# Performance work log

Hardware: AMD Instinct MI355X
Metric: run time of the kernel (lower is better)

The kernel has to match this reference:

```python
import jax, jax.numpy as jnp
import numpy as np


def setup_inputs() -> dict:
    key = jax.random.key(0)
    kx, kf = jax.random.split(key)
    x = jax.random.normal(kx, (4, 8192, 1024), dtype=jnp.float32)
    filt = jax.random.normal(kf, (2048,), dtype=jnp.float32)
    return {"x": x, "filt": filt}


def reference(x, filt):
    # x: (batch, seq, dim); filt: (filter_length,)
    batch, seq, dim = x.shape
    L = filt.shape[0]
    pad = seq + L - 1
    # long-sequence FFT branch (seq > 64)
    xt = jnp.swapaxes(x, 1, 2)                 # (b, d, s)
    fx = jnp.fft.rfft(xt, n=pad, axis=-1)      # (b, d, pad//2+1) complex
    ff = jnp.fft.rfft(filt[::-1], n=pad)       # (pad//2+1,) complex
    conv = jnp.fft.irfft(fx * ff, n=pad, axis=-1)  # (b, d, pad)
    conv = conv[:, :, L - 1:L - 1 + seq]       # valid region, length seq
    return jnp.swapaxes(conv, 1, 2)            # (b, s, d)
```

## Files before the change

kernel.cpp:

```cpp
#include <hip/hip_runtime.h>

typedef unsigned short u16;
typedef unsigned int   u32;

#define BATCH 4
#define SEQ   8192
#define DIM   1024
#define FL    2048
#define TROW  10240

#define BM 512
#define BN 64
#define BK 64
#define NSTAGE 40
#define WOFF 64
#define NW   2272
#define WIN_HI 2174

typedef float  f32x4  __attribute__((ext_vector_type(4)));
typedef __bf16 bf16x8 __attribute__((ext_vector_type(8)));
typedef short  s16x8  __attribute__((ext_vector_type(8)));

typedef const __attribute__((address_space(1))) void* gas_t;
typedef __attribute__((address_space(3))) void* las_t;

__device__ __forceinline__ u16 f2bf(float f) {
  u32 u = __float_as_uint(f);
  u += 0x7fffu + ((u >> 16) & 1u);
  return (u16)(u >> 16);
}

__global__ __launch_bounds__(256) void k_transpose(const float* __restrict__ x,
                                                   u16* __restrict__ xT) {
  __shared__ __align__(16) u16 sm[64 * 66];
  const int bid = blockIdx.x;
  const int tb = bid % (TROW / 64);
  const int db = (bid / (TROW / 64)) % (DIM / 64);
  const int b  = bid / ((TROW / 64) * (DIM / 64));
  const int t0 = tb * 64, d0 = db * 64;
  const int tid = threadIdx.x;

  const int c4 = tid & 15;
  const int lt = tid >> 4;
  const float* xb = x + (size_t)b * SEQ * DIM + d0 + c4 * 4;
  #pragma unroll
  for (int s = 0; s < 64; s += 16) {
    const int tl = lt + s;
    const int t = t0 + tl;
    float4 v = make_float4(0.f, 0.f, 0.f, 0.f);
    if (t < SEQ) v = *(const float4*)(xb + (size_t)t * DIM);
    u32 p0 = (u32)f2bf(v.x) | ((u32)f2bf(v.y) << 16);
    u32 p1 = (u32)f2bf(v.z) | ((u32)f2bf(v.w) << 16);
    u32* dst = (u32*)&sm[tl * 66 + c4 * 4];
    dst[0] = p0;
    dst[1] = p1;
  }
  __syncthreads();
  const int q  = tid & 7;
  const int dl = tid >> 3;
  u16* xo = xT + ((size_t)b * DIM + d0) * TROW + t0 + 8 * q;
  #pragma unroll
  for (int s = 0; s < 2; ++s) {
    const int d = dl + 32 * s;
    u32 w[4];
    #pragma unroll
    for (int h = 0; h < 4; ++h) {
      w[h] = (u32)sm[(8 * q + 2 * h) * 66 + d] |
             ((u32)sm[(8 * q + 2 * h + 1) * 66 + d] << 16);
    }
    *(uint4*)(xo + (size_t)d * TROW) = *(const uint4*)w;
  }
}

__global__ __launch_bounds__(256, 2) void k_conv(const u16* __restrict__ xT,
                                                 const float* __restrict__ filt,
                                                 float* __restrict__ out) {
  __shared__ __align__(16) u16 Wb[NW * 8];
  __shared__ __align__(16) u16 Xs[2][BN * BK];

  const int bid = blockIdx.x;
  const int tb = bid & 15;
  const int db = (bid >> 4) & 15;
  const int b  = bid >> 8;
  const int t0 = tb * BM;
  const int d0 = db * BN;

  const int tid  = threadIdx.x;
  const int wid  = tid >> 6;
  const int lane = tid & 63;
  const int quad = lane >> 4;
  const int lq   = lane & 15;
  const int Tw   = wid * 128;

  for (int w = tid; w < NW; w += 256) {
    const int base = w - WOFF;
    u32 pk[4];
    #pragma unroll
    for (int h = 0; h < 4; ++h) {
      const int i0 = base + 2 * h;
      const int i1 = i0 + 1;
      const float v0 = (i0 >= 0 && i0 < FL) ? filt[i0] : 0.f;
      const float v1 = (i1 >= 0 && i1 < FL) ? filt[i1] : 0.f;
      pk[h] = (u32)f2bf(v0) | ((u32)f2bf(v1) << 16);
    }
    u32* dst = (u32*)&Wb[w * 8];
    dst[0] = pk[0]; dst[1] = pk[1]; dst[2] = pk[2]; dst[3] = pk[3];
  }

  const u16* xrow = xT + ((size_t)b * DIM + d0) * TROW + t0;
  const int p0 = wid * 128 + lane;
  const int p1 = p0 + 64;
  const int ds0 = p0 >> 3, kc0 = (p0 & 7) ^ (ds0 & 7);
  const int ds1 = p1 >> 3, kc1 = (p1 & 7) ^ (ds1 & 7);
  const u16* gp0 = xrow + (size_t)ds0 * TROW + kc0 * 8;
  const u16* gp1 = xrow + (size_t)ds1 * TROW + kc1 * 8;

  f32x4 acc[8][4];
  const f32x4 fz = {0.f, 0.f, 0.f, 0.f};
  #pragma unroll
  for (int i = 0; i < 8; ++i)
    #pragma unroll
    for (int j = 0; j < 4; ++j) acc[i][j] = fz;

  const s16x8 sz = {0, 0, 0, 0, 0, 0, 0, 0};
  bf16x8 roll0 = __builtin_bit_cast(bf16x8, sz);
  bf16x8 roll1 = roll0, roll2 = roll0, roll3 = roll0, roll4 = roll0, roll5 = roll0;

  const int wconst = quad * 8 - Tw - lq + WOFF;
  const int kkLo = Tw - 31;
  const int kkHi = Tw + WIN_HI;

  {
    u16* nb = &Xs[0][wid * 1024];
    __builtin_amdgcn_global_load_lds((gas_t)gp0, (las_t)nb, 16, 0, 0);
    __builtin_amdgcn_global_load_lds((gas_t)gp1, (las_t)(nb + 512), 16, 0, 0);
  }

  for (int st = 0; st < NSTAGE; ++st) {
    __syncthreads();
    if (st + 1 < NSTAGE) {
      const int kkn = (st + 1) * BK;
      u16* nb = &Xs[(st + 1) & 1][wid * 1024];
      __builtin_amdgcn_global_load_lds((gas_t)(gp0 + kkn), (las_t)nb, 16, 0, 0);
      __builtin_amdgcn_global_load_lds((gas_t)(gp1 + kkn), (las_t)(nb + 512), 16, 0, 0);
    }
    const u16* Xc = &Xs[st & 1][0];
    const int kk0 = st * BK;
    #pragma unroll
    for (int half = 0; half < 2; ++half) {
      const int kk = kk0 + half * 32;
      if (kk >= kkLo && kk <= kkHi) {
        bf16x8 bfr[4];
        #pragma unroll
        for (int nt = 0; nt < 4; ++nt) {
          const int dl = nt * 16 + lq;
          const int kc = (half * 4 + quad) ^ (dl & 7);
          bfr[nt] = *(const bf16x8*)&Xc[(dl * 8 + kc) * 8];
        }
        const int w0 = kk + wconst;
        const bf16x8 a0 = *(const bf16x8*)&Wb[w0 * 8];
        const bf16x8 a1 = *(const bf16x8*)&Wb[(w0 - 16) * 8];
        #pragma unroll
        for (int nt = 0; nt < 4; ++nt) {
          acc[0][nt] = __builtin_amdgcn_mfma_f32_16x16x32_bf16(a0,    bfr[nt], acc[0][nt], 0, 0, 0);
          acc[1][nt] = __builtin_amdgcn_mfma_f32_16x16x32_bf16(a1,    bfr[nt], acc[1][nt], 0, 0, 0);
          acc[2][nt] = __builtin_amdgcn_mfma_f32_16x16x32_bf16(roll0, bfr[nt], acc[2][nt], 0, 0, 0);
          acc[3][nt] = __builtin_amdgcn_mfma_f32_16x16x32_bf16(roll1, bfr[nt], acc[3][nt], 0, 0, 0);
          acc[4][nt] = __builtin_amdgcn_mfma_f32_16x16x32_bf16(roll2, bfr[nt], acc[4][nt], 0, 0, 0);
          acc[5][nt] = __builtin_amdgcn_mfma_f32_16x16x32_bf16(roll3, bfr[nt], acc[5][nt], 0, 0, 0);
          acc[6][nt] = __builtin_amdgcn_mfma_f32_16x16x32_bf16(roll4, bfr[nt], acc[6][nt], 0, 0, 0);
          acc[7][nt] = __builtin_amdgcn_mfma_f32_16x16x32_bf16(roll5, bfr[nt], acc[7][nt], 0, 0, 0);
        }
        roll5 = roll3; roll4 = roll2; roll3 = roll1; roll2 = roll0;
        roll1 = a1; roll0 = a0;
      }
    }
  }

  float* ob = out + ((size_t)b * SEQ + t0 + Tw) * DIM + d0;
  #pragma unroll
  for (int mt = 0; mt < 8; ++mt) {
    #pragma unroll
    for (int nt = 0; nt < 4; ++nt) {
      #pragma unroll
      for (int r = 0; r < 4; ++r) {
        ob[(size_t)(mt * 16 + quad * 4 + r) * DIM + nt * 16 + lq] = acc[mt][nt][r];
      }
    }
  }
}

extern "C" void kernel_launch(void* const* d_in, const int* in_sizes, int n_in,
                              void* d_out, int out_size, void* d_ws, size_t ws_size,
                              hipStream_t stream) {
  const float* x    = (const float*)d_in[0];
  const float* filt = (const float*)d_in[1];
  float* out = (float*)d_out;
  u16* xT = (u16*)d_ws;
  (void)in_sizes; (void)n_in; (void)out_size; (void)ws_size;

  k_transpose<<<BATCH * (TROW / 64) * (DIM / 64), 256, 0, stream>>>(x, xT);
  k_conv<<<BATCH * 16 * 16, 256, 0, stream>>>(xT, filt, out);
}
```

Measured before the change: 344.6 us.

## Load B fragments directly from global into registers, drop LDS staging and barriers

Replaces the LDS double-buffered global_load_lds pipeline for the transposed input with per-wave direct global loads into registers, software-pipelined two steps ahead. Each wave now iterates only over its own 68 valid k-steps instead of checking a window across the whole block range, removing per-stage __syncthreads and LDS reads. MFMA bursts are wrapped in s_setprio. The risk is that global loads now expose latency and 16-byte row-strided accesses per lane may coalesce less well than the shared staging did.

```diff
diff --git a/kernel.cpp b/kernel.cpp
--- a/kernel.cpp
+++ b/kernel.cpp
@@ -11,18 +11,13 @@
 
 #define BM 512
 #define BN 64
-#define BK 64
-#define NSTAGE 40
+#define NSTEP 68
 #define WOFF 64
 #define NW   2272
-#define WIN_HI 2174
 
 typedef float  f32x4  __attribute__((ext_vector_type(4)));
 typedef __bf16 bf16x8 __attribute__((ext_vector_type(8)));
 typedef short  s16x8  __attribute__((ext_vector_type(8)));
-
-typedef const __attribute__((address_space(1))) void* gas_t;
-typedef __attribute__((address_space(3))) void* las_t;
 
 __device__ __forceinline__ u16 f2bf(float f) {
   u32 u = __float_as_uint(f);
@@ -76,7 +71,6 @@
                                                  const float* __restrict__ filt,
                                                  float* __restrict__ out) {
   __shared__ __align__(16) u16 Wb[NW * 8];
-  __shared__ __align__(16) u16 Xs[2][BN * BK];
 
   const int bid = blockIdx.x;
   const int tb = bid & 15;
@@ -106,14 +100,12 @@
     u32* dst = (u32*)&Wb[w * 8];
     dst[0] = pk[0]; dst[1] = pk[1]; dst[2] = pk[2]; dst[3] = pk[3];
   }
-
-  const u16* xrow = xT + ((size_t)b * DIM + d0) * TROW + t0;
-  const int p0 = wid * 128 + lane;
-  const int p1 = p0 + 64;
-  const int ds0 = p0 >> 3, kc0 = (p0 & 7) ^ (ds0 & 7);
-  const int ds1 = p1 >> 3, kc1 = (p1 & 7) ^ (ds1 & 7);
-  const u16* gp0 = xrow + (size_t)ds0 * TROW + kc0 * 8;
-  const u16* gp1 = xrow + (size_t)ds1 * TROW + kc1 * 8;
+  __syncthreads();
+
+  const u16* pB0 = xT + ((size_t)b * DIM + d0 + 0 * 16 + lq) * TROW + t0 + Tw + quad * 8;
+  const u16* pB1 = pB0 + (size_t)16 * TROW;
+  const u16* pB2 = pB1 + (size_t)16 * TROW;
+  const u16* pB3 = pB2 + (size_t)16 * TROW;
 
   f32x4 acc[8][4];
   const f32x4 fz = {0.f, 0.f, 0.f, 0.f};
@@ -126,56 +118,72 @@
   bf16x8 roll0 = __builtin_bit_cast(bf16x8, sz);
   bf16x8 roll1 = roll0, roll2 = roll0, roll3 = roll0, roll4 = roll0, roll5 = roll0;
 
-  const int wconst = quad * 8 - Tw - lq + WOFF;
-  const int kkLo = Tw - 31;
-  const int kkHi = Tw + WIN_HI;
-
-  {
-    u16* nb = &Xs[0][wid * 1024];
-    __builtin_amdgcn_global_load_lds((gas_t)gp0, (las_t)nb, 16, 0, 0);
-    __builtin_amdgcn_global_load_lds((gas_t)gp1, (las_t)(nb + 512), 16, 0, 0);
-  }
-
-  for (int st = 0; st < NSTAGE; ++st) {
-    __syncthreads();
-    if (st + 1 < NSTAGE) {
-      const int kkn = (st + 1) * BK;
-      u16* nb = &Xs[(st + 1) & 1][wid * 1024];
-      __builtin_amdgcn_global_load_lds((gas_t)(gp0 + kkn), (las_t)nb, 16, 0, 0);
-      __builtin_amdgcn_global_load_lds((gas_t)(gp1 + kkn), (las_t)(nb + 512), 16, 0, 0);
-    }
-    const u16* Xc = &Xs[st & 1][0];
-    const int kk0 = st * BK;
-    #pragma unroll
-    for (int half = 0; half < 2; ++half) {
-      const int kk = kk0 + half * 32;
-      if (kk >= kkLo && kk <= kkHi) {
-        bf16x8 bfr[4];
-        #pragma unroll
-        for (int nt = 0; nt < 4; ++nt) {
-          const int dl = nt * 16 + lq;
-          const int kc = (half * 4 + quad) ^ (dl & 7);
-          bfr[nt] = *(const bf16x8*)&Xc[(dl * 8 + kc) * 8];
-        }
-        const int w0 = kk + wconst;
-        const bf16x8 a0 = *(const bf16x8*)&Wb[w0 * 8];
-        const bf16x8 a1 = *(const bf16x8*)&Wb[(w0 - 16) * 8];
-        #pragma unroll
-        for (int nt = 0; nt < 4; ++nt) {
-          acc[0][nt] = __builtin_amdgcn_mfma_f32_16x16x32_bf16(a0,    bfr[nt], acc[0][nt], 0, 0, 0);
-          acc[1][nt] = __builtin_amdgcn_mfma_f32_16x16x32_bf16(a1,    bfr[nt], acc[1][nt], 0, 0, 0);
-          acc[2][nt] = __builtin_amdgcn_mfma_f32_16x16x32_bf16(roll0, bfr[nt], acc[2][nt], 0, 0, 0);
-          acc[3][nt] = __builtin_amdgcn_mfma_f32_16x16x32_bf16(roll1, bfr[nt], acc[3][nt], 0, 0, 0);
-          acc[4][nt] = __builtin_amdgcn_mfma_f32_16x16x32_bf16(roll2, bfr[nt], acc[4][nt], 0, 0, 0);
-          acc[5][nt] = __builtin_amdgcn_mfma_f32_16x16x32_bf16(roll3, bfr[nt], acc[5][nt], 0, 0, 0);
-          acc[6][nt] = __builtin_amdgcn_mfma_f32_16x16x32_bf16(roll4, bfr[nt], acc[6][nt], 0, 0, 0);
-          acc[7][nt] = __builtin_amdgcn_mfma_f32_16x16x32_bf16(roll5, bfr[nt], acc[7][nt], 0, 0, 0);
-        }
-        roll5 = roll3; roll4 = roll2; roll3 = roll1; roll2 = roll0;
-        roll1 = a1; roll0 = a0;
-      }
-    }
-  }
+  const int wbase = quad * 8 - lq + WOFF;
+
+#define CONV_STEP(B0, B1, B2, B3, S)                                                   \
+  do {                                                                                 \
+    const int w0_ = (S) * 32 + wbase;                                                  \
+    const bf16x8 a0_ = *(const bf16x8*)&Wb[w0_ * 8];                                   \
+    const bf16x8 a1_ = *(const bf16x8*)&Wb[(w0_ - 16) * 8];                            \
+    __builtin_amdgcn_s_setprio(1);                                                     \
+    acc[0][0] = __builtin_amdgcn_mfma_f32_16x16x32_bf16(a0_,   B0, acc[0][0], 0, 0, 0);\
+    acc[1][0] = __builtin_amdgcn_mfma_f32_16x16x32_bf16(a1_,   B0, acc[1][0], 0, 0, 0);\
+    acc[2][0] = __builtin_amdgcn_mfma_f32_16x16x32_bf16(roll0, B0, acc[2][0], 0, 0, 0);\
+    acc[3][0] = __builtin_amdgcn_mfma_f32_16x16x32_bf16(roll1, B0, acc[3][0], 0, 0, 0);\
+    acc[4][0] = __builtin_amdgcn_mfma_f32_16x16x32_bf16(roll2, B0, acc[4][0], 0, 0, 0);\
+    acc[5][0] = __builtin_amdgcn_mfma_f32_16x16x32_bf16(roll3, B0, acc[5][0], 0, 0, 0);\
+    acc[6][0] = __builtin_amdgcn_mfma_f32_16x16x32_bf16(roll4, B0, acc[6][0], 0, 0, 0);\
+    acc[7][0] = __builtin_amdgcn_mfma_f32_16x16x32_bf16(roll5, B0, acc[7][0], 0, 0, 0);\
+    acc[0][1] = __builtin_amdgcn_mfma_f32_16x16x32_bf16(a0_,   B1, acc[0][1], 0, 0, 0);\
+    acc[1][1] = __builtin_amdgcn_mfma_f32_16x16x32_bf16(a1_,   B1, acc[1][1], 0, 0, 0);\
+    acc[2][1] = __builtin_amdgcn_mfma_f32_16x16x32_bf16(roll0, B1, acc[2][1], 0, 0, 0);\
+    acc[3][1] = __builtin_amdgcn_mfma_f32_16x16x32_bf16(roll1, B1, acc[3][1], 0, 0, 0);\
+    acc[4][1] = __builtin_amdgcn_mfma_f32_16x16x32_bf16(roll2, B1, acc[4][1], 0, 0, 0);\
+    acc[5][1] = __builtin_amdgcn_mfma_f32_16x16x32_bf16(roll3, B1, acc[5][1], 0, 0, 0);\
+    acc[6][1] = __builtin_amdgcn_mfma_f32_16x16x32_bf16(roll4, B1, acc[6][1], 0, 0, 0);\
+    acc[7][1] = __builtin_amdgcn_mfma_f32_16x16x32_bf16(roll5, B1, acc[7][1], 0, 0, 0);\
+    acc[0][2] = __builtin_amdgcn_mfma_f32_16x16x32_bf16(a0_,   B2, acc[0][2], 0, 0, 0);\
+    acc[1][2] = __builtin_amdgcn_mfma_f32_16x16x32_bf16(a1_,   B2, acc[1][2], 0, 0, 0);\
+    acc[2][2] = __builtin_amdgcn_mfma_f32_16x16x32_bf16(roll0, B2, acc[2][2], 0, 0, 0);\
+    acc[3][2] = __builtin_amdgcn_mfma_f32_16x16x32_bf16(roll1, B2, acc[3][2], 0, 0, 0);\
+    acc[4][2] = __builtin_amdgcn_mfma_f32_16x16x32_bf16(roll2, B2, acc[4][2], 0, 0, 0);\
+    acc[5][2] = __builtin_amdgcn_mfma_f32_16x16x32_bf16(roll3, B2, acc[5][2], 0, 0, 0);\
+    acc[6][2] = __builtin_amdgcn_mfma_f32_16x16x32_bf16(roll4, B2, acc[6][2], 0, 0, 0);\
+    acc[7][2] = __builtin_amdgcn_mfma_f32_16x16x32_bf16(roll5, B2, acc[7][2], 0, 0, 0);\
+    acc[0][3] = __builtin_amdgcn_mfma_f32_16x16x32_bf16(a0_,   B3, acc[0][3], 0, 0, 0);\
+    acc[1][3] = __builtin_amdgcn_mfma_f32_16x16x32_bf16(a1_,   B3, acc[1][3], 0, 0, 0);\
+    acc[2][3] = __builtin_amdgcn_mfma_f32_16x16x32_bf16(roll0, B3, acc[2][3], 0, 0, 0);\
+    acc[3][3] = __builtin_amdgcn_mfma_f32_16x16x32_bf16(roll1, B3, acc[3][3], 0, 0, 0);\
+    acc[4][3] = __builtin_amdgcn_mfma_f32_16x16x32_bf16(roll2, B3, acc[4][3], 0, 0, 0);\
+    acc[5][3] = __builtin_amdgcn_mfma_f32_16x16x32_bf16(roll3, B3, acc[5][3], 0, 0, 0);\
+    acc[6][3] = __builtin_amdgcn_mfma_f32_16x16x32_bf16(roll4, B3, acc[6][3], 0, 0, 0);\
+    acc[7][3] = __builtin_amdgcn_mfma_f32_16x16x32_bf16(roll5, B3, acc[7][3], 0, 0, 0);\
+    __builtin_amdgcn_s_setprio(0);                                                     \
+    roll5 = roll3; roll4 = roll2; roll3 = roll1; roll2 = roll0;                        \
+    roll1 = a1_;   roll0 = a0_;                                                        \
+  } while (0)
+
+  bf16x8 bA0 = *(const bf16x8*)(pB0);
+  bf16x8 bA1 = *(const bf16x8*)(pB1);
+  bf16x8 bA2 = *(const bf16x8*)(pB2);
+  bf16x8 bA3 = *(const bf16x8*)(pB3);
+  bf16x8 bB0, bB1, bB2, bB3;
+
+  for (int s = 0; s < NSTEP; s += 2) {
+    bB0 = *(const bf16x8*)(pB0 + (s + 1) * 32);
+    bB1 = *(const bf16x8*)(pB1 + (s + 1) * 32);
+    bB2 = *(const bf16x8*)(pB2 + (s + 1) * 32);
+    bB3 = *(const bf16x8*)(pB3 + (s + 1) * 32);
+    CONV_STEP(bA0, bA1, bA2, bA3, s);
+    if (s + 2 < NSTEP) {
+      bA0 = *(const bf16x8*)(pB0 + (s + 2) * 32);
+      bA1 = *(const bf16x8*)(pB1 + (s + 2) * 32);
+      bA2 = *(const bf16x8*)(pB2 + (s + 2) * 32);
+      bA3 = *(const bf16x8*)(pB3 + (s + 2) * 32);
+    }
+    CONV_STEP(bB0, bB1, bB2, bB3, s + 1);
+  }
+#undef CONV_STEP
 
   float* ob = out + ((size_t)b * SEQ + t0 + Tw) * DIM + d0;
   #pragma unroll
```

After: 374.3 us. 1.09x slower.
